# Kernel optimization log

Hardware: AMD Instinct MI355X
Metric: run time of the kernel (lower is better)

The kernel has to match this reference:

```python
import jax, jax.numpy as jnp
import numpy as np

IN_DIM = 64
HIDDEN = 128
NUM_LAYERS = 2
N_NODES = 10000
N_EDGES = 160000
N_GRAPHS = 32


def _lin_params(key, fan_in, fan_out):
    kw, kb = jax.random.split(key)
    s = 1.0 / np.sqrt(fan_in)
    W = jax.random.uniform(kw, (fan_in, fan_out), jnp.float32, -s, s)
    b = jax.random.uniform(kb, (fan_out,), jnp.float32, -s, s)
    return W, b


def setup_inputs() -> dict:
    key = jax.random.key(0)
    ks = jax.random.split(key, 24)
    H = HIDDEN
    inp = {}
    inp["x1"] = jax.random.normal(ks[0], (N_NODES, IN_DIM), jnp.float32)
    inp["edge_index1"] = jax.random.randint(ks[1], (2, N_EDGES), 0, N_NODES)
    inp["batch1"] = jnp.sort(jax.random.randint(ks[2], (N_NODES,), 0, N_GRAPHS))
    inp["x2"] = jax.random.normal(ks[3], (N_NODES, IN_DIM), jnp.float32)
    inp["edge_index2"] = jax.random.randint(ks[4], (2, N_EDGES), 0, N_NODES)
    inp["batch2"] = jnp.sort(jax.random.randint(ks[5], (N_NODES,), 0, N_GRAPHS))
    # embedding: Linear(in_dim -> hidden)
    inp["W_emb"], inp["b_emb"] = _lin_params(ks[6], IN_DIM, H)
    # per-layer GEMBConv params, stacked over layers
    mW1, mb1, mW2, mb2, uW1, ub1, uW2, ub2 = [], [], [], [], [], [], [], []
    for l in range(NUM_LAYERS):
        k = jax.random.split(ks[7 + l], 4)
        W, b = _lin_params(k[0], 2 * H, 2 * H); mW1.append(W); mb1.append(b)
        W, b = _lin_params(k[1], 2 * H, 2 * H); mW2.append(W); mb2.append(b)
        W, b = _lin_params(k[2], 3 * H, 2 * H); uW1.append(W); ub1.append(b)
        W, b = _lin_params(k[3], 2 * H, H); uW2.append(W); ub2.append(b)
    inp["msg_W1"] = jnp.stack(mW1); inp["msg_b1"] = jnp.stack(mb1)
    inp["msg_W2"] = jnp.stack(mW2); inp["msg_b2"] = jnp.stack(mb2)
    inp["upd_W1"] = jnp.stack(uW1); inp["upd_b1"] = jnp.stack(ub1)
    inp["upd_W2"] = jnp.stack(uW2); inp["upd_b2"] = jnp.stack(ub2)
    # readout: node_net Linear(H -> 2H) (use_gate doubles), graph_net Linear(H -> H)
    inp["node_W"], inp["node_b"] = _lin_params(ks[20], H, 2 * H)
    inp["graph_W"], inp["graph_b"] = _lin_params(ks[21], H, H)
    return inp


def _genet_branch(x, edge_index, batch, W_emb, b_emb,
                  msg_W1, msg_b1, msg_W2, msg_b2,
                  upd_W1, upd_b1, upd_W2, upd_b2,
                  node_W, node_b, graph_W, graph_b):
    H = HIDDEN
    h = x @ W_emb + b_emb  # [N, H]
    tgt, src = edge_index[0], edge_index[1]
    for l in range(NUM_LAYERS):
        # gather-concat: (x[src], x[tgt]) -> [E, 2H]
        mi = jnp.concatenate([h[src], h[tgt]], axis=-1)
        m = jax.nn.relu(mi @ msg_W1[l] + msg_b1[l]) @ msg_W2[l] + msg_b2[l]
        agg = jax.ops.segment_sum(m, tgt, num_segments=N_NODES)  # [N, 2H]
        ui = jnp.concatenate([agg, h], axis=-1)  # [N, 3H]
        u = jax.nn.relu(ui @ upd_W1[l] + upd_b1[l]) @ upd_W2[l] + upd_b2[l]
        h = h + u  # residual node update
    nx = h @ node_W + node_b  # [N, 2H]
    gates = jax.nn.sigmoid(nx[:, :H])
    v = nx[:, H:] * gates
    g = jax.ops.segment_sum(v, batch, num_segments=N_GRAPHS)  # sum pool
    return g @ graph_W + graph_b  # [G, H]


def reference(x1, edge_index1, batch1, x2, edge_index2, batch2,
              W_emb, b_emb, msg_W1, msg_b1, msg_W2, msg_b2,
              upd_W1, upd_b1, upd_W2, upd_b2,
              node_W, node_b, graph_W, graph_b):
    args = (W_emb, b_emb, msg_W1, msg_b1, msg_W2, msg_b2,
            upd_W1, upd_b1, upd_W2, upd_b2, node_W, node_b, graph_W, graph_b)
    embed1 = _genet_branch(x1, edge_index1, batch1, *args)
    embed2 = _genet_branch(x2, edge_index2, batch2, *args)
    return (embed1, embed2)
```

## Files before the change

### kernel.cpp

```cpp
#include <hip/hip_runtime.h>

typedef unsigned short u16;
typedef __bf16 bf16x8 __attribute__((ext_vector_type(8)));
typedef float f32x4 __attribute__((ext_vector_type(4)));
typedef unsigned short u16x8 __attribute__((ext_vector_type(8)));

constexpr int NN  = 10000;
constexpr int NE  = 160000;
constexpr int NG  = 32;
constexpr int HD  = 128;

constexpr size_t WT_PQ   = 0;
constexpr size_t WT_M2R  = 262144;
constexpr size_t WT_UPD1 = 524288;
constexpr size_t WT_U1C  = 917504;
constexpr size_t WT_UPD2 = 1310720;
constexpr size_t WT_NODE = 1441792;
constexpr size_t OFF_C2  = 1507328;
constexpr size_t OFF_DEG = 1509376;
constexpr size_t OFF_ST  = 1589376;
constexpr size_t OFF_CUR = 1669440;
constexpr size_t OFF_SRC = 1749440;
constexpr size_t OFF_H   = 3029440;
constexpr size_t OFF_HB  = 13269440;
constexpr size_t OFF_PQ  = 18389440;
constexpr size_t OFF_UI  = 38869440;
constexpr size_t OFF_G   = 54229440;

#define LSTR 40

__device__ inline u16 f2b(float f) {
  unsigned int u = __float_as_uint(f);
  unsigned int r = u + 0x7fffu + ((u >> 16) & 1u);
  return (u16)(r >> 16);
}
__device__ inline float b2f(u16 u) { return __uint_as_float(((unsigned int)u) << 16); }

__global__ __launch_bounds__(256) void k_prep(
    const float* msgW1, const float* msgW2, const float* updW1,
    const float* updW2, const float* nodeW, const float* msgb2,
    u16* tpq, u16* t2r, u16* t3, u16* tu1c, u16* t4, u16* t5,
    float* c2, int* deg, float* g) {
  int idx = blockIdx.x * 256 + threadIdx.x;
  if (idx < 131072) {
    int l = idx >> 16, r = idx & 65535, n = r >> 7, k = r & 127;
    int row = (n < 256) ? k : (128 + k);
    tpq[idx] = f2b(msgW1[l * 65536 + row * 256 + (n & 255)]);
    t2r[idx] = f2b(msgW2[idx]);
  }
  if (idx < 196608) {
    int l = idx / 98304, r = idx % 98304, n = r / 384, k = r % 384;
    t3[idx] = f2b(updW1[l * 98304 + k * 256 + n]);
  }
  if (idx < 65536) {
    int l = idx >> 15, r = idx & 32767, n = r >> 7, k = r & 127;
    tu1c[l * 98304 + n * 384 + 256 + k] = f2b(updW1[l * 98304 + (256 + k) * 256 + n]);
    int n2 = (idx & 32767) >> 8, k2 = idx & 255;
    t4[idx] = f2b(updW2[(idx >> 15) * 32768 + (k2 << 7) + n2]);
  }
  if (idx < 32768) {
    int n = idx >> 7, k = idx & 127;
    t5[idx] = f2b(nodeW[(k << 8) + n]);
  }
  if (idx < 512) {
    int l = idx >> 8, n = idx & 255;
    const float* b2 = msgb2 + l * 256;
    const float* U1 = updW1 + l * 98304 + n;
    float a = 0.f;
    for (int c = 0; c < 256; c++) a += b2[c] * U1[c * 256];
    c2[idx] = a;
  }
  if (idx < 2 * NN) deg[idx] = 0;
  if (idx < 2 * NG * 128) g[idx] = 0.f;
}

__global__ __launch_bounds__(256) void k_deg(const int* ei0, const int* ei1, int* deg) {
  int br = blockIdx.z;
  int e = blockIdx.x * 256 + threadIdx.x;
  if (e >= NE) return;
  const int* tgt = br ? ei1 : ei0;
  atomicAdd(deg + br * NN + tgt[e], 1);
}

__global__ __launch_bounds__(256) void k_scan(const int* deg, int* starts, int* cursor) {
  int br = blockIdx.z;
  const int* d = deg + br * NN;
  int* st = starts + br * (NN + 8);
  int* cu = cursor + br * NN;
  __shared__ int part[257];
  int t = threadIdx.x;
  int c0 = t * 40;
  int s = 0;
  for (int i = 0; i < 40; i++) if (c0 + i < NN) s += d[c0 + i];
  part[t] = s;
  __syncthreads();
  if (t == 0) {
    int run = 0;
    for (int i = 0; i < 256; i++) { int v = part[i]; part[i] = run; run += v; }
    part[256] = run;
  }
  __syncthreads();
  int run = part[t];
  for (int i = 0; i < 40; i++) {
    int n = c0 + i;
    if (n < NN) { st[n] = run; cu[n] = run; run += d[n]; }
  }
  if (t == 255) st[NN] = part[256];
}

__global__ __launch_bounds__(256) void k_scatter(const int* ei0, const int* ei1,
                                                 int* cursor, int* srcs) {
  int br = blockIdx.z;
  int e = blockIdx.x * 256 + threadIdx.x;
  if (e >= NE) return;
  const int* ei = br ? ei1 : ei0;
  int t = ei[e], s = ei[NE + e];
  int pos = atomicAdd(cursor + br * NN + t, 1);
  srcs[br * NE + pos] = s;
}

__device__ __forceinline__ void pq_from_lhb(
    const u16* lhb, const u16* wq, u16* PQ, int m0, int wave, int lane) {
  const int q = lane >> 4, lr = lane & 15;
  f32x4 a3[2][8];
#pragma unroll
  for (int i = 0; i < 2; i++)
#pragma unroll
    for (int j = 0; j < 8; j++) a3[i][j] = (f32x4){0.f, 0.f, 0.f, 0.f};
#pragma unroll
  for (int k0 = 0; k0 < 128; k0 += 32) {
    bf16x8 af[2], bfr[8];
#pragma unroll
    for (int i = 0; i < 2; i++)
      af[i] = *(const bf16x8*)&lhb[(i * 16 + lr) * 136 + k0 + q * 8];
#pragma unroll
    for (int i = 0; i < 8; i++)
      bfr[i] = *(const bf16x8*)(wq + (size_t)(wave * 128 + i * 16 + lr) * 128 + k0 + q * 8);
#pragma unroll
    for (int mi = 0; mi < 2; mi++)
#pragma unroll
      for (int ni = 0; ni < 8; ni++)
        a3[mi][ni] = __builtin_amdgcn_mfma_f32_16x16x32_bf16(af[mi], bfr[ni], a3[mi][ni], 0, 0, 0);
  }
#pragma unroll
  for (int mi = 0; mi < 2; mi++)
#pragma unroll
    for (int rg = 0; rg < 4; rg++) {
      int grow = m0 + mi * 16 + q * 4 + rg;
      if (grow >= NN) continue;
#pragma unroll
      for (int ni = 0; ni < 8; ni++) {
        int col = wave * 128 + ni * 16 + lr;
        PQ[(size_t)grow * 512 + col] = f2b(a3[mi][ni][rg]);
      }
    }
}

__global__ __launch_bounds__(256) void k_embed(
    const float* x1, const float* x2, const float* W, const float* b,
    float* h, u16* h_bf, u16* ui, const u16* wpq0, u16* PQ_all) {
  int br = blockIdx.z;
  const float* x = br ? x2 : x1;
  float* hB = h + (size_t)br * NN * HD;
  u16* hbB = h_bf + (size_t)br * NN * HD;
  u16* uiB = ui + (size_t)br * NN * 384;
  __shared__ float sW[64 * 128];
  __shared__ float sx[32 * 64];
  __shared__ alignas(16) u16 lhb[32 * 136];
  int tid = threadIdx.x;
  for (int i = tid; i < 64 * 128; i += 256) sW[i] = W[i];
  int r0 = blockIdx.x * 32;
  for (int i = tid; i < 32 * 64; i += 256) {
    int r = i >> 6, k = i & 63;
    sx[i] = (r0 + r < NN) ? x[(size_t)(r0 + r) * 64 + k] : 0.f;
  }
  __syncthreads();
  int c = tid & 127;
  int rbase = (tid >> 7) * 16;
  for (int r = rbase; r < rbase + 16; r++) {
    float acc = b[c];
#pragma unroll
    for (int k = 0; k < 64; k++) acc += sx[r * 64 + k] * sW[k * 128 + c];
    int gr = r0 + r;
    u16 bv = f2b(acc);
    lhb[r * 136 + c] = bv;
    if (gr < NN) {
      hB[(size_t)gr * HD + c] = acc;
      hbB[(size_t)gr * HD + c] = bv;
      uiB[(size_t)gr * 384 + 256 + c] = bv;
    }
  }
  __syncthreads();
  pq_from_lhb(lhb, wpq0, PQ_all + (size_t)br * NN * 512, r0, tid >> 6, tid & 63);
}

__global__ __launch_bounds__(256) void k_edge(const u16* PQ, const int* starts,
                                              const int* srcs, const float* b1, u16* ui) {
  int br = blockIdx.z;
  int node = blockIdx.x * 4 + (threadIdx.x >> 6);
  int lane = threadIdx.x & 63;
  int half = lane >> 5;
  int c0 = (lane & 31) * 8;
  const u16* PQb = PQ + (size_t)br * NN * 512;
  const int* st = starts + br * (NN + 8);
  const int* sr = srcs + br * NE;
  u16x8 qr = *(const u16x8*)(PQb + (size_t)node * 512 + 256 + c0);
  float qv[8], acc[8];
#pragma unroll
  for (int j = 0; j < 8; j++) { qv[j] = b2f(qr[j]) + b1[c0 + j]; acc[j] = 0.f; }
  int e0 = st[node], e1 = st[node + 1];
  int mid = e0 + ((e1 - e0 + 1) >> 1);
  int e = half ? mid : e0;
  int ee = half ? e1 : mid;
  for (; e + 3 < ee; e += 4) {
    int s0 = sr[e], s1 = sr[e + 1], s2 = sr[e + 2], s3 = sr[e + 3];
    u16x8 p0 = *(const u16x8*)(PQb + (size_t)s0 * 512 + c0);
    u16x8 p1 = *(const u16x8*)(PQb + (size_t)s1 * 512 + c0);
    u16x8 p2 = *(const u16x8*)(PQb + (size_t)s2 * 512 + c0);
    u16x8 p3 = *(const u16x8*)(PQb + (size_t)s3 * 512 + c0);
#pragma unroll
    for (int j = 0; j < 8; j++) {
      float v0 = b2f(p0[j]) + qv[j];
      float v1 = b2f(p1[j]) + qv[j];
      float v2 = b2f(p2[j]) + qv[j];
      float v3 = b2f(p3[j]) + qv[j];
      acc[j] += (v0 > 0.f ? v0 : 0.f) + (v1 > 0.f ? v1 : 0.f)
              + (v2 > 0.f ? v2 : 0.f) + (v3 > 0.f ? v3 : 0.f);
    }
  }
  for (; e + 1 < ee; e += 2) {
    int s0 = sr[e], s1 = sr[e + 1];
    u16x8 p0 = *(const u16x8*)(PQb + (size_t)s0 * 512 + c0);
    u16x8 p1 = *(const u16x8*)(PQb + (size_t)s1 * 512 + c0);
#pragma unroll
    for (int j = 0; j < 8; j++) {
      float v0 = b2f(p0[j]) + qv[j];
      float v1 = b2f(p1[j]) + qv[j];
      acc[j] += (v0 > 0.f ? v0 : 0.f) + (v1 > 0.f ? v1 : 0.f);
    }
  }
  if (e < ee) {
    int s0 = sr[e];
    u16x8 p0 = *(const u16x8*)(PQb + (size_t)s0 * 512 + c0);
#pragma unroll
    for (int j = 0; j < 8; j++) {
      float v0 = b2f(p0[j]) + qv[j];
      acc[j] += (v0 > 0.f ? v0 : 0.f);
    }
  }
#pragma unroll
  for (int j = 0; j < 8; j++) acc[j] += __shfl_xor(acc[j], 32);
  if (half == 0) {
    u16x8 o;
#pragma unroll
    for (int j = 0; j < 8; j++) o[j] = f2b(acc[j]);
    *(u16x8*)(ui + (size_t)br * NN * 384 + (size_t)node * 384 + c0) = o;
  }
}

struct GemmP {
  const u16* A;   size_t sA;
  int lda;
  const u16* Wt;  size_t sW;
  u16* outb;  size_t s_outb;
  int M, N, K, ldo;
};

__global__ __launch_bounds__(256) void k_gemm(GemmP p) {
  const int br = blockIdx.z;
  const int tid = threadIdx.x;
  const int lane = tid & 63, wave = tid >> 6;
  const int wm = (wave & 1) * 64, wn = (wave >> 1) * 64;
  const int q = lane >> 4, lr = lane & 15;
  const int m0 = blockIdx.x * 128, n0 = blockIdx.y * 128;
  __shared__ alignas(16) u16 lA[128 * LSTR];
  __shared__ alignas(16) u16 lB[128 * LSTR];

  f32x4 acc[4][4];
#pragma unroll
  for (int i = 0; i < 4; i++)
#pragma unroll
    for (int j = 0; j < 4; j++) acc[i][j] = (f32x4){0.f, 0.f, 0.f, 0.f};

  const u16* Abr = p.A + (size_t)br * p.sA;
  const u16* Wbr = p.Wt + (size_t)br * p.sW;

  for (int k0 = 0; k0 < p.K; k0 += 32) {
#pragma unroll
    for (int c = tid; c < 512; c += 256) {
      int r = c >> 2, kc = (c & 3) << 3;
      int gr = m0 + r;
      u16x8 v = {0, 0, 0, 0, 0, 0, 0, 0};
      if (gr < p.M) v = *(const u16x8*)(Abr + (size_t)gr * p.lda + k0 + kc);
      *(u16x8*)&lA[r * LSTR + kc] = v;
    }
#pragma unroll
    for (int c = tid; c < 512; c += 256) {
      int r = c >> 2, kc = (c & 3) << 3;
      *(u16x8*)&lB[r * LSTR + kc] = *(const u16x8*)(Wbr + (size_t)(n0 + r) * p.K + k0 + kc);
    }
    __syncthreads();
    bf16x8 af[4], bfr[4];
#pragma unroll
    for (int i = 0; i < 4; i++) af[i] = *(const bf16x8*)&lA[(wm + i * 16 + lr) * LSTR + q * 8];
#pragma unroll
    for (int i = 0; i < 4; i++) bfr[i] = *(const bf16x8*)&lB[(wn + i * 16 + lr) * LSTR + q * 8];
#pragma unroll
    for (int mi = 0; mi < 4; mi++)
#pragma unroll
      for (int ni = 0; ni < 4; ni++)
        acc[mi][ni] = __builtin_amdgcn_mfma_f32_16x16x32_bf16(af[mi], bfr[ni], acc[mi][ni], 0, 0, 0);
    __syncthreads();
  }

  u16* ob = p.outb + (size_t)br * p.s_outb;
#pragma unroll
  for (int mi = 0; mi < 4; mi++)
#pragma unroll
    for (int rg = 0; rg < 4; rg++) {
      int row = m0 + wm + mi * 16 + q * 4 + rg;
      if (row >= p.M) continue;
#pragma unroll
      for (int ni = 0; ni < 4; ni++) {
        int col = n0 + wn + ni * 16 + lr;
        ob[(size_t)row * p.ldo + col] = f2b(acc[mi][ni][rg]);
      }
    }
}

__global__ __launch_bounds__(256, 4) void k_upd(
    const u16* ui_all, const u16* w1c, const float* b1u, const float* c2l,
    const int* deg_all, const u16* w2, const float* b2u,
    float* h_all, u16* hb_all, int mode,
    const u16* wpq_next, u16* PQ_all,
    const u16* wnode, const float* nb, const int* b0v, const int* b1v, float* g) {
  const int br = blockIdx.z;
  const int tid = threadIdx.x;
  const int lane = tid & 63, wave = tid >> 6;
  const int q = lane >> 4, lr = lane & 15;
  const int m0 = blockIdx.x * 32;

  __shared__ alignas(16) u16 lA[32 * 392];
  __shared__ alignas(16) u16 lhb[32 * 136];
  __shared__ int sbat[32];
  u16* lU = lA;

  const u16* ui = ui_all + (size_t)br * NN * 384;

  for (int c = tid; c < 1536; c += 256) {
    int r = c / 48, kc = (c % 48) * 8;
    int gr = m0 + r;
    u16x8 v = {0, 0, 0, 0, 0, 0, 0, 0};
    if (gr < NN) v = *(const u16x8*)(ui + (size_t)gr * 384 + kc);
    *(u16x8*)&lA[r * 392 + kc] = v;
  }
  if (mode == 1 && tid < 32) {
    const int* batch = br ? b1v : b0v;
    int n = m0 + tid;
    sbat[tid] = (n < NN) ? batch[n] : -1;
  }
  __syncthreads();

  const int wn = wave * 64;
  f32x4 acc[2][4];
#pragma unroll
  for (int i = 0; i < 2; i++)
#pragma unroll
    for (int j = 0; j < 4; j++) acc[i][j] = (f32x4){0.f, 0.f, 0.f, 0.f};

#pragma unroll
  for (int k0 = 0; k0 < 384; k0 += 32) {
    bf16x8 af[2], bfr[4];
#pragma unroll
    for (int i = 0; i < 2; i++)
      af[i] = *(const bf16x8*)&lA[(i * 16 + lr) * 392 + k0 + q * 8];
#pragma unroll
    for (int i = 0; i < 4; i++)
      bfr[i] = *(const bf16x8*)(w1c + (size_t)(wn + i * 16 + lr) * 384 + k0 + q * 8);
#pragma unroll
    for (int mi = 0; mi < 2; mi++)
#pragma unroll
      for (int ni = 0; ni < 4; ni++)
        acc[mi][ni] = __builtin_amdgcn_mfma_f32_16x16x32_bf16(af[mi], bfr[ni], acc[mi][ni], 0, 0, 0);
  }
  __syncthreads();

  const int* deg = deg_all + br * NN;
#pragma unroll
  for (int mi = 0; mi < 2; mi++)
#pragma unroll
    for (int rg = 0; rg < 4; rg++) {
      int row = mi * 16 + q * 4 + rg;
      int gr = m0 + row;
      float d = (gr < NN) ? (float)deg[gr] : 0.f;
#pragma unroll
      for (int ni = 0; ni < 4; ni++) {
        int col = wn + ni * 16 + lr;
        float v = acc[mi][ni][rg] + b1u[col] + d * c2l[col];
        if (v < 0.f) v = 0.f;
        lU[row * 272 + col] = f2b(v);
      }
    }
  __syncthreads();

  const int wn2 = wave * 32;
  f32x4 acc2[2][2];
#pragma unroll
  for (int i = 0; i < 2; i++)
#pragma unroll
    for (int j = 0; j < 2; j++) acc2[i][j] = (f32x4){0.f, 0.f, 0.f, 0.f};

#pragma unroll
  for (int k0 = 0; k0 < 256; k0 += 32) {
    bf16x8 af[2], bfr[2];
#pragma unroll
    for (int i = 0; i < 2; i++)
      af[i] = *(const bf16x8*)&lU[(i * 16 + lr) * 272 + k0 + q * 8];
#pragma unroll
    for (int i = 0; i < 2; i++)
      bfr[i] = *(const bf16x8*)(w2 + (size_t)(wn2 + i * 16 + lr) * 256 + k0 + q * 8);
#pragma unroll
    for (int mi = 0; mi < 2; mi++)
#pragma unroll
      for (int ni = 0; ni < 2; ni++)
        acc2[mi][ni] = __builtin_amdgcn_mfma_f32_16x16x32_bf16(af[mi], bfr[ni], acc2[mi][ni], 0, 0, 0);
  }

  float* h = h_all + (size_t)br * NN * 128;
  u16* hb = hb_all + (size_t)br * NN * 128;
  u16* uiw = (u16*)ui_all + (size_t)br * NN * 384;
#pragma unroll
  for (int mi = 0; mi < 2; mi++)
#pragma unroll
    for (int rg = 0; rg < 4; rg++) {
      int lrow = mi * 16 + q * 4 + rg;
      int grow = m0 + lrow;
#pragma unroll
      for (int ni = 0; ni < 2; ni++) {
        int col = wn2 + ni * 16 + lr;
        if (grow < NN) {
          size_t o = (size_t)grow * 128 + col;
          float nh = h[o] + acc2[mi][ni][rg] + b2u[col];
          u16 bv = f2b(nh);
          h[o] = nh;
          hb[o] = bv;
          uiw[(size_t)grow * 384 + 256 + col] = bv;
          lhb[lrow * 136 + col] = bv;
        } else {
          lhb[lrow * 136 + col] = 0;
        }
      }
    }
  __syncthreads();

  if (mode == 0) {
    pq_from_lhb(lhb, wpq_next, PQ_all + (size_t)br * NN * 512, m0, wave, lane);
  } else {
    const int wg = wave * 32;
    f32x4 a3[2][4];
#pragma unroll
    for (int i = 0; i < 2; i++)
#pragma unroll
      for (int j = 0; j < 4; j++) a3[i][j] = (f32x4){0.f, 0.f, 0.f, 0.f};
#pragma unroll
    for (int k0 = 0; k0 < 128; k0 += 32) {
      bf16x8 af[2], bfr[4];
#pragma unroll
      for (int i = 0; i < 2; i++)
        af[i] = *(const bf16x8*)&lhb[(i * 16 + lr) * 136 + k0 + q * 8];
#pragma unroll
      for (int i = 0; i < 4; i++) {
        int nrow = (i < 2) ? (wg + i * 16 + lr) : (128 + wg + (i - 2) * 16 + lr);
        bfr[i] = *(const bf16x8*)(wnode + (size_t)nrow * 128 + k0 + q * 8);
      }
#pragma unroll
      for (int mi = 0; mi < 2; mi++)
#pragma unroll
        for (int ni = 0; ni < 4; ni++)
          a3[mi][ni] = __builtin_amdgcn_mfma_f32_16x16x32_bf16(af[mi], bfr[ni], a3[mi][ni], 0, 0, 0);
    }
    float* gb = g + (size_t)br * NG * 128;
    float racc[2] = {0.f, 0.f};
    int cur = -1;
#pragma unroll
    for (int mi = 0; mi < 2; mi++)
#pragma unroll
      for (int rg = 0; rg < 4; rg++) {
        int lrow = mi * 16 + q * 4 + rg;
        int bt = sbat[lrow];
        if (bt != cur) {
          if (cur >= 0) {
#pragma unroll
            for (int ni = 0; ni < 2; ni++)
              atomicAdd(gb + (size_t)cur * 128 + wg + ni * 16 + lr, racc[ni]);
          }
          cur = bt;
          racc[0] = 0.f; racc[1] = 0.f;
        }
        if (bt >= 0) {
#pragma unroll
          for (int ni = 0; ni < 2; ni++) {
            int gcol = wg + ni * 16 + lr;
            float gt = a3[mi][ni][rg] + nb[gcol];
            float vl = a3[mi][ni + 2][rg] + nb[128 + gcol];
            racc[ni] += vl / (1.f + __expf(-gt));
          }
        }
      }
    if (cur >= 0) {
#pragma unroll
      for (int ni = 0; ni < 2; ni++)
        atomicAdd(gb + (size_t)cur * 128 + wg + ni * 16 + lr, racc[ni]);
    }
  }
}

__global__ __launch_bounds__(128) void k_final(const float* g, const float* W,
                                               const float* b, float* out) {
  int br = blockIdx.z, gi = blockIdx.x, j = threadIdx.x;
  __shared__ float sg[128];
  sg[j] = g[(size_t)br * NG * 128 + (size_t)gi * 128 + j];
  __syncthreads();
  float acc = b[j];
#pragma unroll
  for (int k = 0; k < 128; k++) acc += sg[k] * W[k * 128 + j];
  out[(size_t)br * NG * 128 + (size_t)gi * 128 + j] = acc;
}

extern "C" void kernel_launch(void* const* d_in, const int* in_sizes, int n_in,
                              void* d_out, int out_size, void* d_ws, size_t ws_size,
                              hipStream_t stream) {
  const float* x1     = (const float*)d_in[0];
  const int*   ei1    = (const int*)d_in[1];
  const int*   bat1   = (const int*)d_in[2];
  const float* x2     = (const float*)d_in[3];
  const int*   ei2    = (const int*)d_in[4];
  const int*   bat2   = (const int*)d_in[5];
  const float* W_emb  = (const float*)d_in[6];
  const float* b_emb  = (const float*)d_in[7];
  const float* msg_W1 = (const float*)d_in[8];
  const float* msg_b1 = (const float*)d_in[9];
  const float* msg_W2 = (const float*)d_in[10];
  const float* msg_b2 = (const float*)d_in[11];
  const float* upd_W1 = (const float*)d_in[12];
  const float* upd_b1 = (const float*)d_in[13];
  const float* upd_W2 = (const float*)d_in[14];
  const float* upd_b2 = (const float*)d_in[15];
  const float* node_W = (const float*)d_in[16];
  const float* node_b = (const float*)d_in[17];
  const float* graph_W = (const float*)d_in[18];
  const float* graph_b = (const float*)d_in[19];
  float* out = (float*)d_out;

  char* ws = (char*)d_ws;
  u16* wt_pq   = (u16*)(ws + WT_PQ);
  u16* wt_m2r  = (u16*)(ws + WT_M2R);
  u16* wt_upd1 = (u16*)(ws + WT_UPD1);
  u16* wt_u1c  = (u16*)(ws + WT_U1C);
  u16* wt_upd2 = (u16*)(ws + WT_UPD2);
  u16* wt_node = (u16*)(ws + WT_NODE);
  float* c2    = (float*)(ws + OFF_C2);
  int* deg    = (int*)(ws + OFF_DEG);
  int* starts = (int*)(ws + OFF_ST);
  int* cursor = (int*)(ws + OFF_CUR);
  int* srcs   = (int*)(ws + OFF_SRC);
  float* h  = (float*)(ws + OFF_H);
  u16*   hb = (u16*)(ws + OFF_HB);
  u16*   PQ = (u16*)(ws + OFF_PQ);
  u16*   ui = (u16*)(ws + OFF_UI);
  float* g  = (float*)(ws + OFF_G);

  k_prep<<<768, 256, 0, stream>>>(msg_W1, msg_W2, upd_W1, upd_W2, node_W, msg_b2,
                                  wt_pq, wt_m2r, wt_upd1, wt_u1c, wt_upd2, wt_node,
                                  c2, deg, g);
  {
    GemmP pc{};
    pc.A = wt_upd1; pc.sA = 98304; pc.lda = 384;
    pc.Wt = wt_m2r; pc.sW = 65536;
    pc.outb = wt_u1c; pc.s_outb = 98304;
    pc.M = 256; pc.N = 256; pc.K = 256; pc.ldo = 384;
    k_gemm<<<dim3(2, 2, 2), 256, 0, stream>>>(pc);
  }
  k_deg<<<dim3(625, 1, 2), 256, 0, stream>>>(ei1, ei2, deg);
  k_scan<<<dim3(1, 1, 2), 256, 0, stream>>>(deg, starts, cursor);
  k_scatter<<<dim3(625, 1, 2), 256, 0, stream>>>(ei1, ei2, cursor, srcs);
  k_embed<<<dim3(313, 1, 2), 256, 0, stream>>>(x1, x2, W_emb, b_emb, h, hb, ui,
                                               wt_pq, PQ);

  for (int l = 0; l < 2; l++) {
    k_edge<<<dim3(2500, 1, 2), 256, 0, stream>>>(PQ, starts, srcs, msg_b1 + l * 256, ui);

    k_upd<<<dim3(313, 1, 2), 256, 0, stream>>>(
        ui, wt_u1c + (size_t)l * 98304, upd_b1 + l * 256, c2 + l * 256,
        deg, wt_upd2 + (size_t)l * 32768, upd_b2 + l * 128, h, hb,
        (l == 0) ? 0 : 1,
        wt_pq + 65536, PQ,
        wt_node, node_b, bat1, bat2, g);
  }

  k_final<<<dim3(NG, 1, 2), 128, 0, stream>>>(g, graph_W, graph_b, out);
}
```

Baseline: 351.0 us.

## Use MFMA for embedding, fold weight-product GEMM into prep, prefetch B fragments

The scalar FP32 embedding GEMM is replaced with a bf16 MFMA version. A prep pass now converts x1/x2 and W_emb to bf16, and the separate k_gemm launch that built the fused msgW2·updW1 weight is removed, with that product computed inside k_prep by direct dot products. Global B-fragment loads in pq_from_lhb and both k_upd GEMM loops are double-buffered in registers so the next k-step's loads are issued before the current MFMAs. The trade-off is an extra bf16 conversion pass over the inputs, a slow 256-long serial dot product per prepped weight element, and a lower-precision embedding.

```diff
diff --git a/kernel.cpp b/kernel.cpp
--- a/kernel.cpp
+++ b/kernel.cpp
@@ -11,8 +11,6 @@
 constexpr int HD  = 128;
 
 constexpr size_t WT_PQ   = 0;
-constexpr size_t WT_M2R  = 262144;
-constexpr size_t WT_UPD1 = 524288;
 constexpr size_t WT_U1C  = 917504;
 constexpr size_t WT_UPD2 = 1310720;
 constexpr size_t WT_NODE = 1441792;
@@ -26,6 +24,8 @@
 constexpr size_t OFF_PQ  = 18389440;
 constexpr size_t OFF_UI  = 38869440;
 constexpr size_t OFF_G   = 54229440;
+constexpr size_t OFF_XB  = 54262208;
+constexpr size_t WT_EMB  = 56822208;
 
 #define LSTR 40
 
@@ -39,18 +39,14 @@
 __global__ __launch_bounds__(256) void k_prep(
     const float* msgW1, const float* msgW2, const float* updW1,
     const float* updW2, const float* nodeW, const float* msgb2,
-    u16* tpq, u16* t2r, u16* t3, u16* tu1c, u16* t4, u16* t5,
+    const float* W_emb, const float* x1, const float* x2,
+    u16* tpq, u16* tu1c, u16* t4, u16* t5, u16* temb, u16* xb,
     float* c2, int* deg, float* g) {
   int idx = blockIdx.x * 256 + threadIdx.x;
   if (idx < 131072) {
     int l = idx >> 16, r = idx & 65535, n = r >> 7, k = r & 127;
     int row = (n < 256) ? k : (128 + k);
     tpq[idx] = f2b(msgW1[l * 65536 + row * 256 + (n & 255)]);
-    t2r[idx] = f2b(msgW2[idx]);
-  }
-  if (idx < 196608) {
-    int l = idx / 98304, r = idx % 98304, n = r / 384, k = r % 384;
-    t3[idx] = f2b(updW1[l * 98304 + k * 256 + n]);
   }
   if (idx < 65536) {
     int l = idx >> 15, r = idx & 32767, n = r >> 7, k = r & 127;
@@ -72,6 +68,27 @@
   }
   if (idx < 2 * NN) deg[idx] = 0;
   if (idx < 2 * NG * 128) g[idx] = 0.f;
+  if (idx >= 131072 && idx < 262144) {
+    int j = idx - 131072;
+    int l = j >> 16, r = j & 65535, k = r >> 8, n = r & 255;
+    const float* w2p = msgW2 + l * 65536 + k * 256;
+    const float* u1p = updW1 + l * 98304 + n;
+    float a = 0.f;
+    for (int c = 0; c < 256; c++) a += w2p[c] * u1p[c * 256];
+    tu1c[l * 98304 + n * 384 + k] = f2b(a);
+  }
+  if (idx >= 262144 && idx < 270336) {
+    int j = idx - 262144;
+    int n = j >> 6, k = j & 63;
+    temb[j] = f2b(W_emb[(k << 7) + n]);
+  }
+  if (idx >= 270336 && idx < 1550336) {
+    int j = idx - 270336;
+    int br = j >= NN * 64;
+    int jj = br ? j - NN * 64 : j;
+    const float* x = br ? x2 : x1;
+    xb[(size_t)br * NN * 64 + jj] = f2b(x[jj]);
+  }
 }
 
 __global__ __launch_bounds__(256) void k_deg(const int* ei0, const int* ei1, int* deg) {
@@ -127,20 +144,28 @@
   for (int i = 0; i < 2; i++)
 #pragma unroll
     for (int j = 0; j < 8; j++) a3[i][j] = (f32x4){0.f, 0.f, 0.f, 0.f};
+  bf16x8 bcur[8], bnxt[8];
+#pragma unroll
+  for (int i = 0; i < 8; i++)
+    bcur[i] = *(const bf16x8*)(wq + (size_t)(wave * 128 + i * 16 + lr) * 128 + q * 8);
 #pragma unroll
   for (int k0 = 0; k0 < 128; k0 += 32) {
-    bf16x8 af[2], bfr[8];
+    if (k0 + 32 < 128) {
+#pragma unroll
+      for (int i = 0; i < 8; i++)
+        bnxt[i] = *(const bf16x8*)(wq + (size_t)(wave * 128 + i * 16 + lr) * 128 + k0 + 32 + q * 8);
+    }
+    bf16x8 af[2];
 #pragma unroll
     for (int i = 0; i < 2; i++)
       af[i] = *(const bf16x8*)&lhb[(i * 16 + lr) * 136 + k0 + q * 8];
 #pragma unroll
-    for (int i = 0; i < 8; i++)
-      bfr[i] = *(const bf16x8*)(wq + (size_t)(wave * 128 + i * 16 + lr) * 128 + k0 + q * 8);
-#pragma unroll
     for (int mi = 0; mi < 2; mi++)
 #pragma unroll
       for (int ni = 0; ni < 8; ni++)
-        a3[mi][ni] = __builtin_amdgcn_mfma_f32_16x16x32_bf16(af[mi], bfr[ni], a3[mi][ni], 0, 0, 0);
+        a3[mi][ni] = __builtin_amdgcn_mfma_f32_16x16x32_bf16(af[mi], bcur[ni], a3[mi][ni], 0, 0, 0);
+#pragma unroll
+    for (int i = 0; i < 8; i++) bcur[i] = bnxt[i];
   }
 #pragma unroll
   for (int mi = 0; mi < 2; mi++)
@@ -157,41 +182,76 @@
 }
 
 __global__ __launch_bounds__(256) void k_embed(
-    const float* x1, const float* x2, const float* W, const float* b,
+    const u16* xb_all, const u16* wemb, const float* b,
     float* h, u16* h_bf, u16* ui, const u16* wpq0, u16* PQ_all) {
-  int br = blockIdx.z;
-  const float* x = br ? x2 : x1;
+  const int br = blockIdx.z;
+  const int tid = threadIdx.x;
+  const int lane = tid & 63, wave = tid >> 6;
+  const int q = lane >> 4, lr = lane & 15;
+  const int m0 = blockIdx.x * 32;
+
+  __shared__ alignas(16) u16 lx[32 * 72];
+  __shared__ alignas(16) u16 lhb[32 * 136];
+
+  const u16* xb = xb_all + (size_t)br * NN * 64;
+  {
+    int r = tid >> 3, kc = (tid & 7) * 8;
+    int gr = m0 + r;
+    u16x8 v = {0, 0, 0, 0, 0, 0, 0, 0};
+    if (gr < NN) v = *(const u16x8*)(xb + (size_t)gr * 64 + kc);
+    *(u16x8*)&lx[r * 72 + kc] = v;
+  }
+  __syncthreads();
+
+  const int wn = wave * 32;
+  f32x4 acc[2][2];
+#pragma unroll
+  for (int i = 0; i < 2; i++)
+#pragma unroll
+    for (int j = 0; j < 2; j++) acc[i][j] = (f32x4){0.f, 0.f, 0.f, 0.f};
+
+#pragma unroll
+  for (int k0 = 0; k0 < 64; k0 += 32) {
+    bf16x8 af[2], bfr[2];
+#pragma unroll
+    for (int i = 0; i < 2; i++)
+      af[i] = *(const bf16x8*)&lx[(i * 16 + lr) * 72 + k0 + q * 8];
+#pragma unroll
+    for (int i = 0; i < 2; i++)
+      bfr[i] = *(const bf16x8*)(wemb + (size_t)(wn + i * 16 + lr) * 64 + k0 + q * 8);
+#pragma unroll
+    for (int mi = 0; mi < 2; mi++)
+#pragma unroll
+      for (int ni = 0; ni < 2; ni++)
+        acc[mi][ni] = __builtin_amdgcn_mfma_f32_16x16x32_bf16(af[mi], bfr[ni], acc[mi][ni], 0, 0, 0);
+  }
+
   float* hB = h + (size_t)br * NN * HD;
   u16* hbB = h_bf + (size_t)br * NN * HD;
   u16* uiB = ui + (size_t)br * NN * 384;
-  __shared__ float sW[64 * 128];
-  __shared__ float sx[32 * 64];
-  __shared__ alignas(16) u16 lhb[32 * 136];
-  int tid = threadIdx.x;
-  for (int i = tid; i < 64 * 128; i += 256) sW[i] = W[i];
-  int r0 = blockIdx.x * 32;
-  for (int i = tid; i < 32 * 64; i += 256) {
-    int r = i >> 6, k = i & 63;
-    sx[i] = (r0 + r < NN) ? x[(size_t)(r0 + r) * 64 + k] : 0.f;
-  }
-  __syncthreads();
-  int c = tid & 127;
-  int rbase = (tid >> 7) * 16;
-  for (int r = rbase; r < rbase + 16; r++) {
-    float acc = b[c];
-#pragma unroll
-    for (int k = 0; k < 64; k++) acc += sx[r * 64 + k] * sW[k * 128 + c];
-    int gr = r0 + r;
-    u16 bv = f2b(acc);
-    lhb[r * 136 + c] = bv;
-    if (gr < NN) {
-      hB[(size_t)gr * HD + c] = acc;
-      hbB[(size_t)gr * HD + c] = bv;
-      uiB[(size_t)gr * 384 + 256 + c] = bv;
-    }
-  }
-  __syncthreads();
-  pq_from_lhb(lhb, wpq0, PQ_all + (size_t)br * NN * 512, r0, tid >> 6, tid & 63);
+#pragma unroll
+  for (int mi = 0; mi < 2; mi++)
+#pragma unroll
+    for (int rg = 0; rg < 4; rg++) {
+      int lrow = mi * 16 + q * 4 + rg;
+      int gr = m0 + lrow;
+#pragma unroll
+      for (int ni = 0; ni < 2; ni++) {
+        int col = wn + ni * 16 + lr;
+        if (gr < NN) {
+          float nh = acc[mi][ni][rg] + b[col];
+          u16 bv = f2b(nh);
+          hB[(size_t)gr * HD + col] = nh;
+          hbB[(size_t)gr * HD + col] = bv;
+          uiB[(size_t)gr * 384 + 256 + col] = bv;
+          lhb[lrow * 136 + col] = bv;
+        } else {
+          lhb[lrow * 136 + col] = 0;
+        }
+      }
+    }
+  __syncthreads();
+  pq_from_lhb(lhb, wpq0, PQ_all + (size_t)br * NN * 512, m0, wave, lane);
 }
 
 __global__ __launch_bounds__(256) void k_edge(const u16* PQ, const int* starts,
@@ -258,76 +318,6 @@
   }
 }
 
-struct GemmP {
-  const u16* A;   size_t sA;
-  int lda;
-  const u16* Wt;  size_t sW;
-  u16* outb;  size_t s_outb;
-  int M, N, K, ldo;
-};
-
-__global__ __launch_bounds__(256) void k_gemm(GemmP p) {
-  const int br = blockIdx.z;
-  const int tid = threadIdx.x;
-  const int lane = tid & 63, wave = tid >> 6;
-  const int wm = (wave & 1) * 64, wn = (wave >> 1) * 64;
-  const int q = lane >> 4, lr = lane & 15;
-  const int m0 = blockIdx.x * 128, n0 = blockIdx.y * 128;
-  __shared__ alignas(16) u16 lA[128 * LSTR];
-  __shared__ alignas(16) u16 lB[128 * LSTR];
-
-  f32x4 acc[4][4];
-#pragma unroll
-  for (int i = 0; i < 4; i++)
-#pragma unroll
-    for (int j = 0; j < 4; j++) acc[i][j] = (f32x4){0.f, 0.f, 0.f, 0.f};
-
-  const u16* Abr = p.A + (size_t)br * p.sA;
-  const u16* Wbr = p.Wt + (size_t)br * p.sW;
-
-  for (int k0 = 0; k0 < p.K; k0 += 32) {
-#pragma unroll
-    for (int c = tid; c < 512; c += 256) {
-      int r = c >> 2, kc = (c & 3) << 3;
-      int gr = m0 + r;
-      u16x8 v = {0, 0, 0, 0, 0, 0, 0, 0};
-      if (gr < p.M) v = *(const u16x8*)(Abr + (size_t)gr * p.lda + k0 + kc);
-      *(u16x8*)&lA[r * LSTR + kc] = v;
-    }
-#pragma unroll
-    for (int c = tid; c < 512; c += 256) {
-      int r = c >> 2, kc = (c & 3) << 3;
-      *(u16x8*)&lB[r * LSTR + kc] = *(const u16x8*)(Wbr + (size_t)(n0 + r) * p.K + k0 + kc);
-    }
-    __syncthreads();
-    bf16x8 af[4], bfr[4];
-#pragma unroll
-    for (int i = 0; i < 4; i++) af[i] = *(const bf16x8*)&lA[(wm + i * 16 + lr) * LSTR + q * 8];
-#pragma unroll
-    for (int i = 0; i < 4; i++) bfr[i] = *(const bf16x8*)&lB[(wn + i * 16 + lr) * LSTR + q * 8];
-#pragma unroll
-    for (int mi = 0; mi < 4; mi++)
-#pragma unroll
-      for (int ni = 0; ni < 4; ni++)
-        acc[mi][ni] = __builtin_amdgcn_mfma_f32_16x16x32_bf16(af[mi], bfr[ni], acc[mi][ni], 0, 0, 0);
-    __syncthreads();
-  }
-
-  u16* ob = p.outb + (size_t)br * p.s_outb;
-#pragma unroll
-  for (int mi = 0; mi < 4; mi++)
-#pragma unroll
-    for (int rg = 0; rg < 4; rg++) {
-      int row = m0 + wm + mi * 16 + q * 4 + rg;
-      if (row >= p.M) continue;
-#pragma unroll
-      for (int ni = 0; ni < 4; ni++) {
-        int col = n0 + wn + ni * 16 + lr;
-        ob[(size_t)row * p.ldo + col] = f2b(acc[mi][ni][rg]);
-      }
-    }
-}
-
 __global__ __launch_bounds__(256, 4) void k_upd(
     const u16* ui_all, const u16* w1c, const float* b1u, const float* c2l,
     const int* deg_all, const u16* w2, const float* b2u,
@@ -368,20 +358,28 @@
 #pragma unroll
     for (int j = 0; j < 4; j++) acc[i][j] = (f32x4){0.f, 0.f, 0.f, 0.f};
 
+  bf16x8 bcur[4], bnxt[4];
+#pragma unroll
+  for (int i = 0; i < 4; i++)
+    bcur[i] = *(const bf16x8*)(w1c + (size_t)(wn + i * 16 + lr) * 384 + q * 8);
 #pragma unroll
   for (int k0 = 0; k0 < 384; k0 += 32) {
-    bf16x8 af[2], bfr[4];
+    if (k0 + 32 < 384) {
+#pragma unroll
+      for (int i = 0; i < 4; i++)
+        bnxt[i] = *(const bf16x8*)(w1c + (size_t)(wn + i * 16 + lr) * 384 + k0 + 32 + q * 8);
+    }
+    bf16x8 af[2];
 #pragma unroll
     for (int i = 0; i < 2; i++)
       af[i] = *(const bf16x8*)&lA[(i * 16 + lr) * 392 + k0 + q * 8];
 #pragma unroll
-    for (int i = 0; i < 4; i++)
-      bfr[i] = *(const bf16x8*)(w1c + (size_t)(wn + i * 16 + lr) * 384 + k0 + q * 8);
-#pragma unroll
     for (int mi = 0; mi < 2; mi++)
 #pragma unroll
       for (int ni = 0; ni < 4; ni++)
-        acc[mi][ni] = __builtin_amdgcn_mfma_f32_16x16x32_bf16(af[mi], bfr[ni], acc[mi][ni], 0, 0, 0);
+        acc[mi][ni] = __builtin_amdgcn_mfma_f32_16x16x32_bf16(af[mi], bcur[ni], acc[mi][ni], 0, 0, 0);
+#pragma unroll
+    for (int i = 0; i < 4; i++) bcur[i] = bnxt[i];
   }
   __syncthreads();
 
@@ -410,20 +408,28 @@
 #pragma unroll
     for (int j = 0; j < 2; j++) acc2[i][j] = (f32x4){0.f, 0.f, 0.f, 0.f};
 
+  bf16x8 b2c[2], b2n[2];
+#pragma unroll
+  for (int i = 0; i < 2; i++)
+    b2c[i] = *(const bf16x8*)(w2 + (size_t)(wn2 + i * 16 + lr) * 256 + q * 8);
 #pragma unroll
   for (int k0 = 0; k0 < 256; k0 += 32) {
-    bf16x8 af[2], bfr[2];
+    if (k0 + 32 < 256) {
+#pragma unroll
+      for (int i = 0; i < 2; i++)
+        b2n[i] = *(const bf16x8*)(w2 + (size_t)(wn2 + i * 16 + lr) * 256 + k0 + 32 + q * 8);
+    }
+    bf16x8 af[2];
 #pragma unroll
     for (int i = 0; i < 2; i++)
       af[i] = *(const bf16x8*)&lU[(i * 16 + lr) * 272 + k0 + q * 8];
 #pragma unroll
-    for (int i = 0; i < 2; i++)
-      bfr[i] = *(const bf16x8*)(w2 + (size_t)(wn2 + i * 16 + lr) * 256 + k0 + q * 8);
-#pragma unroll
     for (int mi = 0; mi < 2; mi++)
 #pragma unroll
       for (int ni = 0; ni < 2; ni++)
-        acc2[mi][ni] = __builtin_amdgcn_mfma_f32_16x16x32_bf16(af[mi], bfr[ni], acc2[mi][ni], 0, 0, 0);
+        acc2[mi][ni] = __builtin_amdgcn_mfma_f32_16x16x32_bf16(af[mi], b2c[ni], acc2[mi][ni], 0, 0, 0);
+#pragma unroll
+    for (int i = 0; i < 2; i++) b2c[i] = b2n[i];
   }
 
   float* h = h_all + (size_t)br * NN * 128;
@@ -554,11 +560,11 @@
 
   char* ws = (char*)d_ws;
   u16* wt_pq   = (u16*)(ws + WT_PQ);
-  u16* wt_m2r  = (u16*)(ws + WT_M2R);
-  u16* wt_upd1 = (u16*)(ws + WT_UPD1);
   u16* wt_u1c  = (u16*)(ws + WT_U1C);
   u16* wt_upd2 = (u16*)(ws + WT_UPD2);
   u16* wt_node = (u16*)(ws + WT_NODE);
+  u16* wt_emb  = (u16*)(ws + WT_EMB);
+  u16* xb      = (u16*)(ws + OFF_XB);
   float* c2    = (float*)(ws + OFF_C2);
   int* deg    = (int*)(ws + OFF_DEG);
   int* starts = (int*)(ws + OFF_ST);
@@ -570,21 +576,14 @@
   u16*   ui = (u16*)(ws + OFF_UI);
   float* g  = (float*)(ws + OFF_G);
 
-  k_prep<<<768, 256, 0, stream>>>(msg_W1, msg_W2, upd_W1, upd_W2, node_W, msg_b2,
-                                  wt_pq, wt_m2r, wt_upd1, wt_u1c, wt_upd2, wt_node,
-                                  c2, deg, g);
-  {
-    GemmP pc{};
-    pc.A = wt_upd1; pc.sA = 98304; pc.lda = 384;
-    pc.Wt = wt_m2r; pc.sW = 65536;
-    pc.outb = wt_u1c; pc.s_outb = 98304;
-    pc.M = 256; pc.N = 256; pc.K = 256; pc.ldo = 384;
-    k_gemm<<<dim3(2, 2, 2), 256, 0, stream>>>(pc);
-  }
+  k_prep<<<6057, 256, 0, stream>>>(msg_W1, msg_W2, upd_W1, upd_W2, node_W, msg_b2,
+                                   W_emb, x1, x2,
+                                   wt_pq, wt_u1c, wt_upd2, wt_node, wt_emb, xb,
+                                   c2, deg, g);
   k_deg<<<dim3(625, 1, 2), 256, 0, stream>>>(ei1, ei2, deg);
   k_scan<<<dim3(1, 1, 2), 256, 0, stream>>>(deg, starts, cursor);
   k_scatter<<<dim3(625, 1, 2), 256, 0, stream>>>(ei1, ei2, cursor, srcs);
-  k_embed<<<dim3(313, 1, 2), 256, 0, stream>>>(x1, x2, W_emb, b_emb, h, hb, ui,
+  k_embed<<<dim3(313, 1, 2), 256, 0, stream>>>(xb, wt_emb, b_emb, h, hb, ui,
                                                wt_pq, PQ);
 
   for (int l = 0; l < 2; l++) {
```

New measurement: 331.8 us. 1.06x faster.
